# Performance work log

Measured on AMD Instinct MI355X. Metric: run time of the kernel, lower is better.

## Reference

```python
import jax, jax.numpy as jnp
import numpy as np

B, S, D = 2, 2048, 1024
H, DH = 16, 64  # num_heads, attention_dim


def setup_inputs() -> dict:
    key = jax.random.key(0)
    ks = jax.random.split(key, 10)
    x = jax.random.normal(ks[0], (B, S, D), dtype=jnp.float32)
    # causal mask, broadcast over batch and heads (mask==0 -> -inf)
    mask = jnp.tril(jnp.ones((S, S), dtype=jnp.int32))[None, None]
    s = 1.0 / np.sqrt(D)
    Wq = jax.random.normal(ks[1], (D, H * DH), dtype=jnp.float32) * s
    bq = jnp.zeros((H * DH,), dtype=jnp.float32)
    Wk = jax.random.normal(ks[2], (D, H * DH), dtype=jnp.float32) * s
    bk = jnp.zeros((H * DH,), dtype=jnp.float32)
    Wv = jax.random.normal(ks[3], (D, H * DH), dtype=jnp.float32) * s
    bv = jnp.zeros((H * DH,), dtype=jnp.float32)
    Wo = jax.random.normal(ks[4], (H * DH, D), dtype=jnp.float32) * (1.0 / np.sqrt(H * DH))
    bo = jnp.zeros((D,), dtype=jnp.float32)
    return {"x": x, "mask": mask, "Wq": Wq, "bq": bq, "Wk": Wk, "bk": bk,
            "Wv": Wv, "bv": bv, "Wo": Wo, "bo": bo}


def reference(x, mask, Wq, bq, Wk, bk, Wv, bv, Wo, bo):
    b, s, _ = x.shape
    q = (x @ Wq + bq).reshape(b, s, H, DH)
    k = (x @ Wk + bk).reshape(b, s, H, DH)
    v = (x @ Wv + bv).reshape(b, s, H, DH)
    # scores: [B, H, S, S]
    scores = jnp.einsum("bshd,bthd->bhst", q, k) / jnp.sqrt(jnp.float32(DH))
    scores = jnp.where(mask == 0, -jnp.inf, scores)
    w = jax.nn.softmax(scores, axis=-1)
    attended = jnp.einsum("bhst,bthd->bshd", w, v).reshape(b, s, H * DH)
    return attended @ Wo + bo
```

## Files before the change

### kernel.cpp

```cpp
#include <hip/hip_runtime.h>
#include <hip/hip_bf16.h>

#define B_ 2
#define S_ 2048
#define D_ 1024
#define H_ 16
#define DH_ 64

typedef __attribute__((ext_vector_type(8))) short bf16x8;
typedef __attribute__((ext_vector_type(4))) float f32x4;
typedef __attribute__((ext_vector_type(16))) float f32x16;

#define QSCALE 0.18033688011112042f

__device__ __forceinline__ ushort f2b(float f){
  __hip_bfloat16 h = __float2bfloat16(f);
  return *reinterpret_cast<ushort*>(&h);
}

__device__ __forceinline__ unsigned cvtpk(float lo, float hi){
  unsigned r;
  asm("v_cvt_pk_bf16_f32 %0, %1, %2" : "=v"(r) : "v"(lo), "v"(hi));
  return r;
}

__device__ __forceinline__ void gload16(const ushort* g, ushort* l){
  __builtin_amdgcn_global_load_lds((const __attribute__((address_space(1))) unsigned*)g,
                                   (__attribute__((address_space(3))) unsigned*)l, 16, 0, 0);
}

__global__ __launch_bounds__(256) void k_prep(const float* __restrict__ x, ushort* __restrict__ xb,
                                              const float* __restrict__ Wq, const float* __restrict__ Wk,
                                              const float* __restrict__ Wv, const float* __restrict__ Wo,
                                              ushort* __restrict__ WqkvT, ushort* __restrict__ WoT){
  int bid = blockIdx.x, tid = threadIdx.x;
  if (bid < 2048){
    int i = (bid*256 + tid)*8;
    float4 v0 = *(const float4*)(x + i);
    float4 v1 = *(const float4*)(x + i + 4);
    uint4 o;
    o.x = f2b(v0.x) | ((unsigned)f2b(v0.y)<<16);
    o.y = f2b(v0.z) | ((unsigned)f2b(v0.w)<<16);
    o.z = f2b(v1.x) | ((unsigned)f2b(v1.y)<<16);
    o.w = f2b(v1.z) | ((unsigned)f2b(v1.w)<<16);
    *(uint4*)(xb + i) = o;
    return;
  }
  bid -= 2048;
  const int w = bid >> 10, tb = bid & 1023;
  const float* src = (w==0)?Wq:(w==1)?Wk:(w==2)?Wv:Wo;
  ushort* dst = (w==3)?WoT : WqkvT + (size_t)w*(1024*1024);
  __shared__ float tile[32][33];
  const int bx2 = tb & 31, by2 = tb >> 5;
  const int c0 = bx2*32, r0 = by2*32;
  const int tx = tid & 31, ty = tid >> 5;
  #pragma unroll
  for (int i=0;i<4;i++)
    tile[ty + i*8][tx] = src[(size_t)(r0 + ty + i*8)*1024 + c0 + tx];
  __syncthreads();
  #pragma unroll
  for (int i=0;i<4;i++)
    dst[(size_t)(c0 + ty + i*8)*1024 + r0 + tx] = f2b(tile[tx][ty + i*8]);
}

__global__ __launch_bounds__(512, 4) void k_gemm_qkv(const ushort* __restrict__ A,
                                                     const ushort* __restrict__ BT,
                                                     const float* __restrict__ b0p,
                                                     const float* __restrict__ b1p,
                                                     const float* __restrict__ b2p,
                                                     ushort* __restrict__ Cp,
                                                     int M, int N, int K){
  __shared__ ushort As[256*64];
  __shared__ ushort Bs[128*64];
  const int tid = threadIdx.x;
  const int nbn = N >> 7;
  const int bm = blockIdx.x / nbn, bn = blockIdx.x % nbn;
  const int m0 = bm << 8, n0 = bn << 7;
  const int wave = tid >> 6, lane = tid & 63;
  const int wm = (wave >> 1) << 6, wn = (wave & 1) << 6;
  const int lr = lane & 15, lq = lane >> 4;

  f32x4 acc[4][4] = {};

  const int r0 = tid >> 3;
  const int gk = (tid & 7) ^ (r0 & 7);
  const ushort* Agb = A  + (size_t)(m0 + r0)*K + gk*8;
  const ushort* Bgb = BT + (size_t)(n0 + r0)*K + gk*8;
  const int lofs = tid*8;

  for (int kt = 0; kt < K; kt += 64){
    __syncthreads();
    #pragma unroll
    for (int j=0;j<4;j++)
      gload16(Agb + (size_t)j*64*K + kt, &As[lofs + j*4096]);
    #pragma unroll
    for (int j=0;j<2;j++)
      gload16(Bgb + (size_t)j*64*K + kt, &Bs[lofs + j*4096]);
    __syncthreads();
    #pragma unroll
    for (int kk=0;kk<2;kk++){
      bf16x8 af[4], bfr[4];
      #pragma unroll
      for (int i=0;i<4;i++){
        int ra = wm + i*16 + lr;
        af[i]  = *(bf16x8*)&As[ra*64 + (((kk*4+lq) ^ (ra & 7)) << 3)];
        int rb = wn + i*16 + lr;
        bfr[i] = *(bf16x8*)&Bs[rb*64 + (((kk*4+lq) ^ (rb & 7)) << 3)];
      }
      __builtin_amdgcn_s_setprio(1);
      #pragma unroll
      for (int mi=0;mi<4;mi++)
        #pragma unroll
        for (int ni=0;ni<4;ni++)
          acc[mi][ni] = __builtin_amdgcn_mfma_f32_16x16x32_bf16(af[mi], bfr[ni], acc[mi][ni], 0, 0, 0);
      __builtin_amdgcn_s_setprio(0);
    }
  }

  const int seg = n0 >> 10;
  const float* bp = (seg==0 ? b0p : (seg==1 ? b1p : b2p));
  #pragma unroll
  for (int mi=0;mi<4;mi++){
    #pragma unroll
    for (int ni=0;ni<4;ni++){
      int col = n0 + wn + ni*16 + lr;
      int cl = col & 1023;
      float bv = bp[cl];
      int row0 = m0 + wm + mi*16 + lq*4;
      ushort* Qb = Cp;
      if (seg == 0){
        #pragma unroll
        for (int r=0;r<4;r++)
          Qb[(size_t)(row0+r)*1024 + cl] = f2b((acc[mi][ni][r] + bv) * QSCALE);
      } else if (seg == 1){
        ushort* Kb = Qb + (4u<<20);
        #pragma unroll
        for (int r=0;r<4;r++)
          Kb[(size_t)(row0+r)*1024 + cl] = f2b(acc[mi][ni][r] + bv);
      } else {
        ushort* Vt = Qb + (8u<<20);
        int bb = row0 >> 11, srow = row0 & 2047;
        uint2 pk;
        pk.x = cvtpk(acc[mi][ni][0]+bv, acc[mi][ni][1]+bv);
        pk.y = cvtpk(acc[mi][ni][2]+bv, acc[mi][ni][3]+bv);
        *(uint2*)&Vt[((size_t)(bb*1024 + cl))*2048 + srow] = pk;
      }
    }
  }
}

__global__ __launch_bounds__(256) void k_gemm_out(const ushort* __restrict__ A,
                                                  const ushort* __restrict__ BT,
                                                  const float* __restrict__ bias,
                                                  float* __restrict__ Cp,
                                                  int M, int N, int K){
  __shared__ ushort As[128*64];
  __shared__ ushort Bs[128*64];
  const int tid = threadIdx.x;
  const int nbn = N >> 7;
  const int bm = blockIdx.x / nbn, bn = blockIdx.x % nbn;
  const int m0 = bm << 7, n0 = bn << 7;
  const int wave = tid >> 6, lane = tid & 63;
  const int wm = (wave >> 1) << 6, wn = (wave & 1) << 6;
  const int lr = lane & 15, lq = lane >> 4;

  f32x4 acc[4][4] = {};

  const ushort* Ag[4]; const ushort* Bg[4]; int lofs[4];
  #pragma unroll
  for (int j=0;j<4;j++){
    int c = tid + j*256, row = c >> 3, slot = c & 7;
    int gk2 = slot ^ (row & 7);
    Ag[j] = A  + (size_t)(m0 + row)*K + gk2*8;
    Bg[j] = BT + (size_t)(n0 + row)*K + gk2*8;
    lofs[j] = c*8;
  }

  for (int kt = 0; kt < K; kt += 64){
    __syncthreads();
    #pragma unroll
    for (int j=0;j<4;j++){
      gload16(Ag[j] + kt, &As[lofs[j]]);
      gload16(Bg[j] + kt, &Bs[lofs[j]]);
    }
    __syncthreads();
    #pragma unroll
    for (int kk=0;kk<2;kk++){
      bf16x8 af[4], bfr[4];
      #pragma unroll
      for (int i=0;i<4;i++){
        int ra = wm + i*16 + lr;
        af[i]  = *(bf16x8*)&As[ra*64 + (((kk*4+lq) ^ (ra & 7)) << 3)];
        int rb = wn + i*16 + lr;
        bfr[i] = *(bf16x8*)&Bs[rb*64 + (((kk*4+lq) ^ (rb & 7)) << 3)];
      }
      __builtin_amdgcn_s_setprio(1);
      #pragma unroll
      for (int mi=0;mi<4;mi++)
        #pragma unroll
        for (int ni=0;ni<4;ni++)
          acc[mi][ni] = __builtin_amdgcn_mfma_f32_16x16x32_bf16(af[mi], bfr[ni], acc[mi][ni], 0, 0, 0);
      __builtin_amdgcn_s_setprio(0);
    }
  }

  #pragma unroll
  for (int mi=0;mi<4;mi++){
    #pragma unroll
    for (int ni=0;ni<4;ni++){
      int col = n0 + wn + ni*16 + lr;
      float bv = bias[col];
      int row0 = m0 + wm + mi*16 + lq*4;
      #pragma unroll
      for (int r=0;r<4;r++)
        Cp[(size_t)(row0+r)*N + col] = acc[mi][ni][r] + bv;
    }
  }
}

__global__ __launch_bounds__(128) void k_attn_mfma(const ushort* __restrict__ Qb,
                                                   const ushort* __restrict__ Kb,
                                                   const ushort* __restrict__ Vtg,
                                                   ushort* __restrict__ Ob,
                                                   ushort* __restrict__ accPb,
                                                   float* __restrict__ lP){
  __shared__ ushort Ks[2][64*64];
  __shared__ ushort Vs[2][64*64];
  const int bid = blockIdx.x;
  int bh, qt, t0, NT, half; bool split;
  if (bid < 1024){
    int s = bid >> 5; bh = bid & 31;
    qt = 31 - (s >> 1); half = s & 1; split = true;
    if (half == 0){ t0 = 16; NT = qt; }
    else          { t0 = 0;  NT = 15; }
  } else {
    int s = bid - 1024; qt = 15 - (s >> 5); bh = s & 31;
    t0 = 0; NT = qt; half = 0; split = false;
  }
  const bool diag = (!split) || (half == 0);
  const int h = bh & 15, b = bh >> 4;
  const int q0 = qt << 6;
  const int tid = threadIdx.x;
  const int wq = tid >> 6, lane = tid & 63;
  const int ql = lane & 31, hi = lane >> 5;

  bf16x8 Qf[4];
  {
    const ushort* qp = Qb + (size_t)(b*S_ + q0 + wq*32 + ql)*1024 + h*64 + hi*8;
    #pragma unroll
    for (int dc=0; dc<4; ++dc) Qf[dc] = *(const bf16x8*)(qp + dc*16);
  }

  float lsum = 0.f;
  f32x16 acc0 = {}, acc1 = {};

  const int r0c = tid >> 3, cc = tid & 7;
  const int gk = cc ^ (r0c & 7);
  const ushort* Kp = Kb  + (size_t)(b*S_ + r0c)*1024 + h*64 + gk*8;
  const ushort* Vp = Vtg + (size_t)(bh*64 + r0c)*2048 + gk*8;
  const int lofs = tid*8;

  #define ASTAGE(t, buf) { \
    const ushort* kp_ = Kp + (size_t)(t)*65536; \
    const ushort* vp_ = Vp + (t)*64; \
    gload16(kp_,           &Ks[buf][lofs]); \
    gload16(kp_ + 16*1024, &Ks[buf][lofs+1024]); \
    gload16(kp_ + 32*1024, &Ks[buf][lofs+2048]); \
    gload16(kp_ + 48*1024, &Ks[buf][lofs+3072]); \
    gload16(vp_,           &Vs[buf][lofs]); \
    gload16(vp_ + 16*2048, &Vs[buf][lofs+1024]); \
    gload16(vp_ + 32*2048, &Vs[buf][lofs+2048]); \
    gload16(vp_ + 48*2048, &Vs[buf][lofs+3072]); }

  ASTAGE(t0, 0);
  __syncthreads();
  int cur = 0;
  for (int kt = t0; ; ++kt){
    if (kt < NT) ASTAGE(kt+1, cur^1);

    #pragma unroll
    for (int kg = 0; kg < 2; ++kg){
      f32x16 sf = {};
      const int krow = kg*32 + ql;
      __builtin_amdgcn_s_setprio(1);
      #pragma unroll
      for (int dc = 0; dc < 4; ++dc){
        bf16x8 kf = *(const bf16x8*)((const char*)Ks[cur] + krow*128 + ((dc*32 + hi*16) ^ ((krow & 7) << 4)));
        sf = __builtin_amdgcn_mfma_f32_32x32x16_bf16(kf, Qf[dc], sf, 0, 0, 0);
      }
      __builtin_amdgcn_s_setprio(0);

      float p[16];
      if (diag && kt == NT){
        const int th = q0 + wq*32 + ql - kt*64 - kg*32 - 4*hi;
        #pragma unroll
        for (int r=0;r<16;++r){
          int kin = (r&3) + 8*(r>>2);
          p[r] = exp2f(kin > th ? -1e30f : sf[r]);
        }
      } else {
        #pragma unroll
        for (int r=0;r<16;++r) p[r] = exp2f(sf[r]);
      }
      float s16 = 0.f;
      #pragma unroll
      for (int r=0;r<16;++r) s16 += p[r];
      lsum += s16;

      unsigned w0=cvtpk(p[0],p[1]),   w1=cvtpk(p[2],p[3]);
      unsigned w2=cvtpk(p[4],p[5]),   w3=cvtpk(p[6],p[7]);
      unsigned w4=cvtpk(p[8],p[9]),   w5=cvtpk(p[10],p[11]);
      unsigned w6=cvtpk(p[12],p[13]), w7=cvtpk(p[14],p[15]);
      unsigned z0 = (unsigned)__shfl_xor((int)(hi ? w0 : w2), 32, 64);
      unsigned z1 = (unsigned)__shfl_xor((int)(hi ? w1 : w3), 32, 64);
      unsigned z2 = (unsigned)__shfl_xor((int)(hi ? w4 : w6), 32, 64);
      unsigned z3 = (unsigned)__shfl_xor((int)(hi ? w5 : w7), 32, 64);
      uint4 fa, fb;
      fa.x = hi ? z0 : w0;  fa.y = hi ? z1 : w1;
      fa.z = hi ? w2 : z0;  fa.w = hi ? w3 : z1;
      fb.x = hi ? z2 : w4;  fb.y = hi ? z3 : w5;
      fb.z = hi ? w6 : z2;  fb.w = hi ? w7 : z3;
      bf16x8 pf0 = *(bf16x8*)&fa;
      bf16x8 pf1 = *(bf16x8*)&fb;

      __builtin_amdgcn_s_setprio(1);
      {
        const char* vbase = (const char*)Vs[cur];
        const int vr0 = ql;
        const int vr1 = 32 + ql;
        bf16x8 v00 = *(const bf16x8*)(vbase + vr0*128 + ((kg*64 + hi*16)      ^ ((vr0 & 7) << 4)));
        bf16x8 v01 = *(const bf16x8*)(vbase + vr0*128 + ((kg*64 + 32 + hi*16) ^ ((vr0 & 7) << 4)));
        bf16x8 v10 = *(const bf16x8*)(vbase + vr1*128 + ((kg*64 + hi*16)      ^ ((vr1 & 7) << 4)));
        bf16x8 v11 = *(const bf16x8*)(vbase + vr1*128 + ((kg*64 + 32 + hi*16) ^ ((vr1 & 7) << 4)));
        acc0 = __builtin_amdgcn_mfma_f32_32x32x16_bf16(pf0, v00, acc0, 0, 0, 0);
        acc0 = __builtin_amdgcn_mfma_f32_32x32x16_bf16(pf1, v01, acc0, 0, 0, 0);
        acc1 = __builtin_amdgcn_mfma_f32_32x32x16_bf16(pf0, v10, acc1, 0, 0, 0);
        acc1 = __builtin_amdgcn_mfma_f32_32x32x16_bf16(pf1, v11, acc1, 0, 0, 0);
      }
      __builtin_amdgcn_s_setprio(0);
    }

    if (kt == NT) break;
    __syncthreads();
    cur ^= 1;
  }
  #undef ASTAGE

  float lst = lsum + __shfl_xor(lsum, 32, 64);
  float irv = 1.0f / lst;

  if (!split){
    ushort* Opb = Ob + (size_t)(b*S_)*1024 + h*64;
    #pragma unroll
    for (int r=0;r<16;++r){
      int qr = (r&3) + 8*(r>>2) + 4*hi;
      float ir = __shfl(irv, qr, 64);
      size_t row = (size_t)(q0 + wq*32 + qr);
      Opb[row*1024 + ql]      = f2b(acc0[r] * ir);
      Opb[row*1024 + 32 + ql] = f2b(acc1[r] * ir);
    }
  } else {
    const int slot = (qt - 16)*32 + bh;
    const int rb = half*32768 + slot*64 + wq*32;
    #pragma unroll
    for (int r=0;r<16;++r){
      int qr = (r&3) + 8*(r>>2) + 4*hi;
      float ir = __shfl(irv, qr, 64);
      accPb[(size_t)(rb + qr)*64 + ql]      = f2b(acc0[r] * ir);
      accPb[(size_t)(rb + qr)*64 + 32 + ql] = f2b(acc1[r] * ir);
    }
    if (lane < 32) lP[rb + ql] = lst;
  }
}

__global__ __launch_bounds__(256) void k_combine(const ushort* __restrict__ accPb,
                                                 const float* __restrict__ lP,
                                                 ushort* __restrict__ Ob){
  const int slot = blockIdx.x;
  const int qt = 16 + (slot >> 5), bh = slot & 31;
  const int b = bh >> 4, h = bh & 15;
  const int row = threadIdx.x >> 2, dq = (threadIdx.x & 3) * 16;
  const int trA = slot*64 + row, trB = 32768 + slot*64 + row;
  float lA = lP[trA], lB = lP[trB];
  float inv = 1.0f / (lA + lB);
  float wA = lA * inv, wB = lB * inv;
  const ushort* pa = accPb + (size_t)trA*64 + dq;
  const ushort* pb = accPb + (size_t)trB*64 + dq;
  uint4 a0 = *(const uint4*)pa, a1 = *(const uint4*)(pa + 8);
  uint4 b0 = *(const uint4*)pb, b1 = *(const uint4*)(pb + 8);
  unsigned aw[8] = {a0.x,a0.y,a0.z,a0.w,a1.x,a1.y,a1.z,a1.w};
  unsigned bw[8] = {b0.x,b0.y,b0.z,b0.w,b1.x,b1.y,b1.z,b1.w};
  unsigned ow[8];
  #pragma unroll
  for (int e=0;e<8;e++){
    float alo = __uint_as_float(aw[e] << 16), ahi = __uint_as_float(aw[e] & 0xffff0000u);
    float blo = __uint_as_float(bw[e] << 16), bhi = __uint_as_float(bw[e] & 0xffff0000u);
    ow[e] = cvtpk(alo*wA + blo*wB, ahi*wA + bhi*wB);
  }
  ushort* op = Ob + (size_t)(b*S_ + qt*64 + row)*1024 + h*64 + dq;
  uint4 o0, o1;
  o0.x=ow[0]; o0.y=ow[1]; o0.z=ow[2]; o0.w=ow[3];
  o1.x=ow[4]; o1.y=ow[5]; o1.z=ow[6]; o1.w=ow[7];
  *(uint4*)(op)     = o0;
  *(uint4*)(op + 8) = o1;
}

extern "C" void kernel_launch(void* const* d_in, const int* in_sizes, int n_in,
                              void* d_out, int out_size, void* d_ws, size_t ws_size,
                              hipStream_t stream){
  const float* x  = (const float*)d_in[0];
  const float* Wq = (const float*)d_in[2];
  const float* bq = (const float*)d_in[3];
  const float* Wk = (const float*)d_in[4];
  const float* bk = (const float*)d_in[5];
  const float* Wv = (const float*)d_in[6];
  const float* bv = (const float*)d_in[7];
  const float* Wo = (const float*)d_in[8];
  const float* bo = (const float*)d_in[9];

  char* ws = (char*)d_ws;
  const size_t MB = 1024u*1024u;
  ushort* xb    = (ushort*)(ws + 0);
  ushort* WqkvT = (ushort*)(ws + 8*MB);
  ushort* WoT   = (ushort*)(ws + 14*MB);
  ushort* Qb    = (ushort*)(ws + 16*MB);
  ushort* Kb    = (ushort*)(ws + 24*MB);
  ushort* Vtg   = (ushort*)(ws + 32*MB);
  float*  lP    = (float*)(ws + 40*MB);
  ushort* attb  = xb;
  ushort* accPb = (ushort*)d_out;

  const int MN = B_*S_;

  k_prep<<<dim3(6144), dim3(256), 0, stream>>>(x, xb, Wq, Wk, Wv, Wo, WqkvT, WoT);

  k_gemm_qkv<<<dim3((MN/256)*(3072/128)), dim3(512), 0, stream>>>(xb, WqkvT, bq, bk, bv, Qb, MN, 3072, 1024);

  k_attn_mfma<<<dim3(1536), dim3(128), 0, stream>>>(Qb, Kb, Vtg, attb, accPb, lP);
  k_combine<<<dim3(512), dim3(256), 0, stream>>>(accPb, lP, attb);

  k_gemm_out<<<dim3((MN/128)*(1024/128)), dim3(256), 0, stream>>>(attb, WoT, bo, (float*)d_out, MN, 1024, 1024);
}
```

Before: 119.8 us.

## Use 128-row query blocks with variable KV chunk splits and register-staged loads

The attention kernel now processes 128 query rows per block with 4 waves, and splits the causal KV range into chunks of up to 10 tiles. Long query blocks get 2 to 4 chunks and short ones none, so work is balanced across 1088 blocks. K/V staging moves from direct global-to-LDS loads to register-prefetched loads written into swizzled LDS one tile ahead. The combine kernel merges a variable number of partials. This is meant to reuse each K/V tile across more queries and even out load, at the cost of more partial-result traffic and register pressure.

```diff
diff --git a/kernel.cpp b/kernel.cpp
--- a/kernel.cpp
+++ b/kernel.cpp
@@ -12,6 +12,11 @@
 typedef __attribute__((ext_vector_type(16))) float f32x16;
 
 #define QSCALE 0.18033688011112042f
+
+__device__ __forceinline__ int chunk_off(int qb){
+  return (qb <= 9) ? 2*(qb-5) : (qb <= 14 ? 10 + 3*(qb-10) : 25);
+}
+#define CHUNKS_PER_BH 29
 
 __device__ __forceinline__ ushort f2b(float f){
   __hip_bfloat16 h = __float2bfloat16(f);
@@ -218,7 +223,7 @@
   }
 }
 
-__global__ __launch_bounds__(128) void k_attn_mfma(const ushort* __restrict__ Qb,
+__global__ __launch_bounds__(256) void k_attn_mfma(const ushort* __restrict__ Qb,
                                                    const ushort* __restrict__ Kb,
                                                    const ushort* __restrict__ Vtg,
                                                    ushort* __restrict__ Ob,
@@ -227,19 +232,22 @@
   __shared__ ushort Ks[2][64*64];
   __shared__ ushort Vs[2][64*64];
   const int bid = blockIdx.x;
-  int bh, qt, t0, NT, half; bool split;
-  if (bid < 1024){
-    int s = bid >> 5; bh = bid & 31;
-    qt = 31 - (s >> 1); half = s & 1; split = true;
-    if (half == 0){ t0 = 16; NT = qt; }
-    else          { t0 = 0;  NT = 15; }
-  } else {
-    int s = bid - 1024; qt = 15 - (s >> 5); bh = s & 31;
-    t0 = 0; NT = qt; half = 0; split = false;
-  }
-  const bool diag = (!split) || (half == 0);
+  const int bh = bid & 31;
+  const int j = 33 - (bid >> 5);
+  int qb, c; bool split;
+  if (j < 5){ qb = j; c = 0; split = false; }
+  else {
+    int sc = j - 5;
+    if (sc < 10){ qb = 5 + (sc >> 1); c = sc & 1; }
+    else if (sc < 25){ int t = sc - 10; int q3 = t/3; qb = 10 + q3; c = t - 3*q3; }
+    else { qb = 15; c = sc - 25; }
+    split = true;
+  }
+  const int t0 = c*10;
+  const int NT = min(t0 + 9, 2*qb + 1);
+  const bool diag = (NT == 2*qb + 1);
   const int h = bh & 15, b = bh >> 4;
-  const int q0 = qt << 6;
+  const int q0 = qb << 7;
   const int tid = threadIdx.x;
   const int wq = tid >> 6, lane = tid & 63;
   const int ql = lane & 31, hi = lane >> 5;
@@ -254,29 +262,37 @@
   float lsum = 0.f;
   f32x16 acc0 = {}, acc1 = {};
 
-  const int r0c = tid >> 3, cc = tid & 7;
-  const int gk = cc ^ (r0c & 7);
-  const ushort* Kp = Kb  + (size_t)(b*S_ + r0c)*1024 + h*64 + gk*8;
-  const ushort* Vp = Vtg + (size_t)(bh*64 + r0c)*2048 + gk*8;
-  const int lofs = tid*8;
-
-  #define ASTAGE(t, buf) { \
-    const ushort* kp_ = Kp + (size_t)(t)*65536; \
-    const ushort* vp_ = Vp + (t)*64; \
-    gload16(kp_,           &Ks[buf][lofs]); \
-    gload16(kp_ + 16*1024, &Ks[buf][lofs+1024]); \
-    gload16(kp_ + 32*1024, &Ks[buf][lofs+2048]); \
-    gload16(kp_ + 48*1024, &Ks[buf][lofs+3072]); \
-    gload16(vp_,           &Vs[buf][lofs]); \
-    gload16(vp_ + 16*2048, &Vs[buf][lofs+1024]); \
-    gload16(vp_ + 32*2048, &Vs[buf][lofs+2048]); \
-    gload16(vp_ + 48*2048, &Vs[buf][lofs+3072]); }
-
-  ASTAGE(t0, 0);
+  const int r0c = tid >> 3, sl = tid & 7;
+  const int r1c = r0c + 32;
+  const int wo0 = r0c*64 + ((sl*8) ^ ((r0c & 7) << 3));
+  const int wo1 = r1c*64 + ((sl*8) ^ ((r1c & 7) << 3));
+  const ushort* Kp0 = Kb  + (size_t)(b*S_ + r0c)*1024 + h*64 + sl*8;
+  const ushort* Kp1 = Kb  + (size_t)(b*S_ + r1c)*1024 + h*64 + sl*8;
+  const ushort* Vp0 = Vtg + (size_t)(bh*64 + r0c)*2048 + sl*8;
+  const ushort* Vp1 = Vtg + (size_t)(bh*64 + r1c)*2048 + sl*8;
+
+  uint4 ka, kc, va, vc;
+  #define ALOAD(t) { \
+    ka = *(const uint4*)(Kp0 + (size_t)(t)*65536); \
+    kc = *(const uint4*)(Kp1 + (size_t)(t)*65536); \
+    va = *(const uint4*)(Vp0 + (t)*64); \
+    vc = *(const uint4*)(Vp1 + (t)*64); }
+  #define AWRITE(buf) { \
+    *(uint4*)&Ks[buf][wo0] = ka; \
+    *(uint4*)&Ks[buf][wo1] = kc; \
+    *(uint4*)&Vs[buf][wo0] = va; \
+    *(uint4*)&Vs[buf][wo1] = vc; }
+
+  ALOAD(t0);
+  AWRITE(0);
+  if (t0 + 1 <= NT) ALOAD(t0+1);
   __syncthreads();
   int cur = 0;
   for (int kt = t0; ; ++kt){
-    if (kt < NT) ASTAGE(kt+1, cur^1);
+    if (kt < NT){
+      AWRITE(cur^1);
+      if (kt + 2 <= NT) ALOAD(kt+2);
+    }
 
     #pragma unroll
     for (int kg = 0; kg < 2; ++kg){
@@ -291,7 +307,7 @@
       __builtin_amdgcn_s_setprio(0);
 
       float p[16];
-      if (diag && kt == NT){
+      if (diag && kt >= 2*qb){
         const int th = q0 + wq*32 + ql - kt*64 - kg*32 - 4*hi;
         #pragma unroll
         for (int r=0;r<16;++r){
@@ -344,7 +360,8 @@
     __syncthreads();
     cur ^= 1;
   }
-  #undef ASTAGE
+  #undef ALOAD
+  #undef AWRITE
 
   float lst = lsum + __shfl_xor(lsum, 32, 64);
   float irv = 1.0f / lst;
@@ -360,44 +377,52 @@
       Opb[row*1024 + 32 + ql] = f2b(acc1[r] * ir);
     }
   } else {
-    const int slot = (qt - 16)*32 + bh;
-    const int rb = half*32768 + slot*64 + wq*32;
+    const int slot = bh*CHUNKS_PER_BH + chunk_off(qb) + c;
+    const int rbase = slot*128 + wq*32;
     #pragma unroll
     for (int r=0;r<16;++r){
       int qr = (r&3) + 8*(r>>2) + 4*hi;
       float ir = __shfl(irv, qr, 64);
-      accPb[(size_t)(rb + qr)*64 + ql]      = f2b(acc0[r] * ir);
-      accPb[(size_t)(rb + qr)*64 + 32 + ql] = f2b(acc1[r] * ir);
-    }
-    if (lane < 32) lP[rb + ql] = lst;
-  }
-}
-
-__global__ __launch_bounds__(256) void k_combine(const ushort* __restrict__ accPb,
+      accPb[(size_t)(rbase + qr)*64 + ql]      = f2b(acc0[r] * ir);
+      accPb[(size_t)(rbase + qr)*64 + 32 + ql] = f2b(acc1[r] * ir);
+    }
+    if (lane < 32) lP[rbase + ql] = lst;
+  }
+}
+
+__global__ __launch_bounds__(512) void k_combine(const ushort* __restrict__ accPb,
                                                  const float* __restrict__ lP,
                                                  ushort* __restrict__ Ob){
-  const int slot = blockIdx.x;
-  const int qt = 16 + (slot >> 5), bh = slot & 31;
+  const int bid = blockIdx.x;
+  const int qb = 5 + (bid >> 5), bh = bid & 31;
   const int b = bh >> 4, h = bh & 15;
+  const int nc = (qb <= 9) ? 2 : (qb <= 14 ? 3 : 4);
+  const int base = bh*CHUNKS_PER_BH + chunk_off(qb);
   const int row = threadIdx.x >> 2, dq = (threadIdx.x & 3) * 16;
-  const int trA = slot*64 + row, trB = 32768 + slot*64 + row;
-  float lA = lP[trA], lB = lP[trB];
-  float inv = 1.0f / (lA + lB);
-  float wA = lA * inv, wB = lB * inv;
-  const ushort* pa = accPb + (size_t)trA*64 + dq;
-  const ushort* pb = accPb + (size_t)trB*64 + dq;
-  uint4 a0 = *(const uint4*)pa, a1 = *(const uint4*)(pa + 8);
-  uint4 b0 = *(const uint4*)pb, b1 = *(const uint4*)(pb + 8);
-  unsigned aw[8] = {a0.x,a0.y,a0.z,a0.w,a1.x,a1.y,a1.z,a1.w};
-  unsigned bw[8] = {b0.x,b0.y,b0.z,b0.w,b1.x,b1.y,b1.z,b1.w};
+
+  float w[4];
+  float lt = 0.f;
+  for (int i=0;i<nc;++i){ w[i] = lP[(base+i)*128 + row]; lt += w[i]; }
+  float inv = 1.0f / lt;
+
+  float o[16];
+  #pragma unroll
+  for (int e=0;e<16;++e) o[e] = 0.f;
+  for (int i=0;i<nc;++i){
+    float wi = w[i] * inv;
+    const ushort* p = accPb + (size_t)((base+i)*128 + row)*64 + dq;
+    uint4 a0 = *(const uint4*)p, a1 = *(const uint4*)(p + 8);
+    unsigned aw[8] = {a0.x,a0.y,a0.z,a0.w,a1.x,a1.y,a1.z,a1.w};
+    #pragma unroll
+    for (int e=0;e<8;++e){
+      o[e*2]   += wi * __uint_as_float(aw[e] << 16);
+      o[e*2+1] += wi * __uint_as_float(aw[e] & 0xffff0000u);
+    }
+  }
   unsigned ow[8];
   #pragma unroll
-  for (int e=0;e<8;e++){
-    float alo = __uint_as_float(aw[e] << 16), ahi = __uint_as_float(aw[e] & 0xffff0000u);
-    float blo = __uint_as_float(bw[e] << 16), bhi = __uint_as_float(bw[e] & 0xffff0000u);
-    ow[e] = cvtpk(alo*wA + blo*wB, ahi*wA + bhi*wB);
-  }
-  ushort* op = Ob + (size_t)(b*S_ + qt*64 + row)*1024 + h*64 + dq;
+  for (int e=0;e<8;++e) ow[e] = cvtpk(o[e*2], o[e*2+1]);
+  ushort* op = Ob + (size_t)(b*S_ + qb*128 + row)*1024 + h*64 + dq;
   uint4 o0, o1;
   o0.x=ow[0]; o0.y=ow[1]; o0.z=ow[2]; o0.w=ow[3];
   o1.x=ow[4]; o1.y=ow[5]; o1.z=ow[6]; o1.w=ow[7];
@@ -436,8 +461,8 @@
 
   k_gemm_qkv<<<dim3((MN/256)*(3072/128)), dim3(512), 0, stream>>>(xb, WqkvT, bq, bk, bv, Qb, MN, 3072, 1024);
 
-  k_attn_mfma<<<dim3(1536), dim3(128), 0, stream>>>(Qb, Kb, Vtg, attb, accPb, lP);
-  k_combine<<<dim3(512), dim3(256), 0, stream>>>(accPb, lP, attb);
+  k_attn_mfma<<<dim3(1088), dim3(256), 0, stream>>>(Qb, Kb, Vtg, attb, accPb, lP);
+  k_combine<<<dim3(352), dim3(512), 0, stream>>>(accPb, lP, attb);
 
   k_gemm_out<<<dim3((MN/128)*(1024/128)), dim3(256), 0, stream>>>(attb, WoT, bo, (float*)d_out, MN, 1024, 1024);
 }
```

Result: no change. 118.1 us (-1.4%).
